# Performance work log

Hardware: AMD Instinct MI355X
Metric: run time of the kernel (lower is better)

The kernel has to match this reference:

```python
import jax, jax.numpy as jnp
import numpy as np

D = 768
HID = 4 * D
B = 16
HRES = 32
WRES = 32
T = HRES * WRES


def layernorm(x, g, b, eps=1e-5):
    m = jnp.mean(x, axis=-1, keepdims=True)
    v = jnp.mean(jnp.square(x - m), axis=-1, keepdims=True)
    return (x - m) * jax.lax.rsqrt(v + eps) * g + b


def q_shift(x, H, W):
    # Vision-RWKV quad-directional token shift: split channels into 4 groups,
    # each group takes the neighboring patch's value in one direction (zero pad).
    Bn, N, C = x.shape
    xi = x.reshape(Bn, H, W, C)
    c = C // 4
    g0 = jnp.pad(xi[:, :, :-1, 0 * c:1 * c], ((0, 0), (0, 0), (1, 0), (0, 0)))  # from left
    g1 = jnp.pad(xi[:, :, 1:, 1 * c:2 * c], ((0, 0), (0, 0), (0, 1), (0, 0)))   # from right
    g2 = jnp.pad(xi[:, :-1, :, 2 * c:3 * c], ((0, 0), (1, 0), (0, 0), (0, 0)))  # from above
    g3 = jnp.pad(xi[:, 1:, :, 3 * c:4 * c], ((0, 0), (0, 1), (0, 0), (0, 0)))   # from below
    return jnp.concatenate([g0, g1, g2, g3], axis=-1).reshape(Bn, N, C)


def wkv_scan(w_log, u, k, v):
    # Numerically stable RWKV WKV recurrence (per-channel linear attention).
    # k, v: [B, T, C]; w = -exp(w_log) is the per-channel decay, u the bonus.
    w = -jnp.exp(w_log)
    kT = jnp.swapaxes(k, 0, 1)  # [T, B, C]
    vT = jnp.swapaxes(v, 0, 1)
    Bn, C = k.shape[0], k.shape[2]
    aa0 = jnp.zeros((Bn, C), k.dtype)
    bb0 = jnp.zeros((Bn, C), k.dtype)
    pp0 = jnp.full((Bn, C), -1e30, k.dtype)

    def step(carry, kv):
        aa, bb, pp = carry
        kt, vt = kv
        ww = u + kt
        p = jnp.maximum(pp, ww)
        e1 = jnp.exp(pp - p)
        e2 = jnp.exp(ww - p)
        out = (e1 * aa + e2 * vt) / (e1 * bb + e2)
        ww2 = pp + w
        p2 = jnp.maximum(ww2, kt)
        e1b = jnp.exp(ww2 - p2)
        e2b = jnp.exp(kt - p2)
        return (e1b * aa + e2b * vt, e1b * bb + e2b, p2), out

    _, outT = jax.lax.scan(step, (aa0, bb0, pp0), (kT, vT))
    return jnp.swapaxes(outT, 0, 1)  # [B, T, C]


def setup_inputs() -> dict:
    key = jax.random.key(0)
    ks = jax.random.split(key, 16)

    def nrm(k, shape, s=0.02):
        return jax.random.normal(k, shape, jnp.float32) * s

    return {
        "x": jax.random.normal(ks[0], (B, T, D), jnp.float32),
        "H": HRES,
        "W": WRES,
        "ln1_g": jnp.ones((D,), jnp.float32),
        "ln1_b": jnp.zeros((D,), jnp.float32),
        "ln2_g": jnp.ones((D,), jnp.float32),
        "ln2_b": jnp.zeros((D,), jnp.float32),
        "mu_k": jax.random.uniform(ks[1], (D,), jnp.float32),
        "mu_v": jax.random.uniform(ks[2], (D,), jnp.float32),
        "mu_r": jax.random.uniform(ks[3], (D,), jnp.float32),
        "w_log": nrm(ks[4], (D,), 0.5),
        "u": nrm(ks[5], (D,), 0.5),
        "Wk": nrm(ks[6], (D, D)),
        "Wv": nrm(ks[7], (D, D)),
        "Wr": nrm(ks[8], (D, D)),
        "Wo": nrm(ks[9], (D, D)),
        "cmu_k": jax.random.uniform(ks[10], (D,), jnp.float32),
        "cmu_r": jax.random.uniform(ks[11], (D,), jnp.float32),
        "Ck": nrm(ks[12], (HID, D)),
        "Cv": nrm(ks[13], (D, HID)),
        "Cr": nrm(ks[14], (D, D)),
    }


def reference(x, H, W, ln1_g, ln1_b, ln2_g, ln2_b, mu_k, mu_v, mu_r, w_log, u,
              Wk, Wv, Wr, Wo, cmu_k, cmu_r, Ck, Cv, Cr):
    h = x
    # ---- spatial mix (RWKV time-mix over patch sequence) ----
    a = layernorm(h, ln1_g, ln1_b)
    sx = q_shift(a, H, W)
    xk = a * mu_k + sx * (1.0 - mu_k)
    xv = a * mu_v + sx * (1.0 - mu_v)
    xr = a * mu_r + sx * (1.0 - mu_r)
    k = xk @ Wk.T
    v = xv @ Wv.T
    r = jax.nn.sigmoid(xr @ Wr.T)
    wkv = wkv_scan(w_log, u, k, v)
    h = h + (r * wkv) @ Wo.T
    # ---- channel mix (squared-ReLU gated FFN) ----
    a2 = layernorm(h, ln2_g, ln2_b)
    sx2 = q_shift(a2, H, W)
    xk2 = a2 * cmu_k + sx2 * (1.0 - cmu_k)
    xr2 = a2 * cmu_r + sx2 * (1.0 - cmu_r)
    kk = jnp.square(jax.nn.relu(xk2 @ Ck.T))
    h = h + jax.nn.sigmoid(xr2 @ Cr.T) * (kk @ Cv.T)
    # ---- outer residual from RWKVBlock.forward ----
    return h + x
```

## Files before the change

### kernel.cpp

```cpp
#include <hip/hip_runtime.h>
#include <hip/hip_bf16.h>

#define DD   768
#define TT   1024
#define BBATCH 16
#define NROWS (BBATCH * TT)
#define HIDN 3072
#define HHALF 1536
#define HH 32
#define WW 32
#define DW  (DD * DD)
#define DH  (DD * HIDN)
#define CCH 64
#define PCH (TT / CCH)

typedef float  floatx4 __attribute__((ext_vector_type(4)));
typedef __bf16 bf16x8  __attribute__((ext_vector_type(8)));

__device__ __forceinline__ float bf2f(__hip_bfloat16 v) { return __bfloat162float(v); }
__device__ __forceinline__ __hip_bfloat16 f2bf(float v) { return __float2bfloat16(v); }
__device__ __forceinline__ float toF(__hip_bfloat16 v) { return __bfloat162float(v); }
__device__ __forceinline__ float toF(float v) { return v; }

#define GL2LDS(gp, lp)  __builtin_amdgcn_global_load_lds(                     \
    (const __attribute__((address_space(1))) void*)(gp),                      \
    (__attribute__((address_space(3))) void*)(lp), 16, 0, 0)

__global__ __launch_bounds__(256)
void cvt_k(const float* __restrict__ s, __hip_bfloat16* __restrict__ d, int n)
{
    const int i = (blockIdx.x * 256 + threadIdx.x) * 4;
    if (i >= n) return;
    const float4 v = *reinterpret_cast<const float4*>(s + i);
    __hip_bfloat16 o[4] = {f2bf(v.x), f2bf(v.y), f2bf(v.z), f2bf(v.w)};
    *reinterpret_cast<ushort4*>(d + i) = *reinterpret_cast<const ushort4*>(o);
}

template <typename TIN>
__global__ __launch_bounds__(256)
void ln_stats_k(const TIN* __restrict__ x,
                float* __restrict__ mean, float* __restrict__ rstd)
{
    const int row = blockIdx.x, tid = threadIdx.x;
    const int lane = tid & 63, wid = tid >> 6;
    const TIN* xr = x + (size_t)row * DD;
    float s1 = 0.f, s2 = 0.f;
#pragma unroll
    for (int i = 0; i < 3; ++i) {
        const float v = toF(xr[tid + i * 256]);
        s1 += v; s2 += v * v;
    }
#pragma unroll
    for (int off = 32; off > 0; off >>= 1) {
        s1 += __shfl_down(s1, off);
        s2 += __shfl_down(s2, off);
    }
    __shared__ float sh[8];
    if (lane == 0) { sh[wid] = s1; sh[4 + wid] = s2; }
    __syncthreads();
    if (tid == 0) {
        s1 = sh[0] + sh[1] + sh[2] + sh[3];
        s2 = sh[4] + sh[5] + sh[6] + sh[7];
        const float m = s1 * (1.f / DD);
        mean[row] = m;
        rstd[row] = rsqrtf(s2 * (1.f / DD) - m * m + 1e-5f);
    }
}

template <typename TIN>
__device__ __forceinline__ float ln_at(const TIN* __restrict__ x,
                                       const float* __restrict__ mean,
                                       const float* __restrict__ rstd,
                                       const float* __restrict__ g,
                                       const float* __restrict__ b,
                                       int grow, int c)
{
    return (toF(x[(size_t)grow * DD + c]) - mean[grow]) * rstd[grow] * g[c] + b[c];
}

template <typename TIN, int NOUT>
__global__ __launch_bounds__(256)
void mix_k(const TIN* __restrict__ x,
           const float* __restrict__ mean, const float* __restrict__ rstd,
           const float* __restrict__ g, const float* __restrict__ b,
           const float* __restrict__ muk,
           const float* __restrict__ muv,
           const float* __restrict__ mur,
           __hip_bfloat16* __restrict__ xk,
           __hip_bfloat16* __restrict__ xv,
           __hip_bfloat16* __restrict__ xr)
{
    const size_t idx = (size_t)blockIdx.x * 256 + threadIdx.x;
    const int c  = (int)(idx % DD);
    const int n  = (int)((idx / DD) % TT);
    const int bb = (int)(idx / ((size_t)DD * TT));
    const int y = n >> 5, xp = n & 31;
    const int grow = bb * TT + n;

    const float av = ln_at(x, mean, rstd, g, b, grow, c);

    const int grp = c / (DD / 4);
    int ny = y, nx = xp; bool ok;
    if      (grp == 0) { nx = xp - 1; ok = xp > 0;      }
    else if (grp == 1) { nx = xp + 1; ok = xp < WW - 1; }
    else if (grp == 2) { ny = y - 1;  ok = y > 0;       }
    else               { ny = y + 1;  ok = y < HH - 1;  }
    const float sx = ok ? ln_at(x, mean, rstd, g, b, bb * TT + ny * WW + nx, c) : 0.f;

    const float mk = muk[c], mr = mur[c];
    xk[idx] = f2bf(av * mk + sx * (1.f - mk));
    xr[idx] = f2bf(av * mr + sx * (1.f - mr));
    if (NOUT == 3) {
        const float mv = muv[c];
        xv[idx] = f2bf(av * mv + sx * (1.f - mv));
    }
}

#define BM 128
#define BN 128
#define BKK 64

template <int MODE>
__global__ __launch_bounds__(256, 2)
void gemm_bt(const __hip_bfloat16* __restrict__ A,
             const __hip_bfloat16* __restrict__ W,
             int K, int Wstr, int Nn,
             __hip_bfloat16* __restrict__ outB,
             float* __restrict__ outF,
             const __hip_bfloat16* __restrict__ auxS,
             const __hip_bfloat16* __restrict__ auxH,
             const float* __restrict__ auxX)
{
    __shared__ __align__(16) unsigned short lA[BM * BKK];
    __shared__ __align__(16) unsigned short lB[BN * BKK];

    const int tid  = threadIdx.x;
    const int bm   = blockIdx.x, bn = blockIdx.y;
    const int lane = tid & 63, wid = tid >> 6;
    const int l15  = lane & 15, quad = lane >> 4;
    const int m0   = (wid & 1) * 64;
    const int n0   = (wid >> 1) * 64;

    const int srow  = lane >> 3;
    const int gcolg = (lane & 7) ^ (srow & 7);
    const int s0    = wid * 4;

    floatx4 acc[4][4];
#pragma unroll
    for (int i = 0; i < 4; ++i)
#pragma unroll
        for (int j = 0; j < 4; ++j)
            acc[i][j] = floatx4{0.f, 0.f, 0.f, 0.f};

    const int swzbase = l15 & 7;

    for (int k0 = 0; k0 < K; k0 += BKK) {
#pragma unroll
        for (int t = 0; t < 4; ++t) {
            const int s   = s0 + t;
            const int row = s * 8 + srow;
            GL2LDS(A + (size_t)(bm * BM + row) * K    + k0 + gcolg * 8,
                   &lA[s * 512]);
            GL2LDS(W + (size_t)(bn * BN + row) * Wstr + k0 + gcolg * 8,
                   &lB[s * 512]);
        }
        __syncthreads();
#pragma unroll
        for (int kk = 0; kk < BKK; kk += 32) {
            const int swz = (((kk >> 3) + quad) ^ swzbase) * 8;
            bf16x8 af[4], bfr[4];
#pragma unroll
            for (int i = 0; i < 4; ++i)
                af[i] = *reinterpret_cast<const bf16x8*>(
                    &lA[(m0 + i * 16 + l15) * BKK + swz]);
#pragma unroll
            for (int j = 0; j < 4; ++j)
                bfr[j] = *reinterpret_cast<const bf16x8*>(
                    &lB[(n0 + j * 16 + l15) * BKK + swz]);
#pragma unroll
            for (int i = 0; i < 4; ++i)
#pragma unroll
                for (int j = 0; j < 4; ++j)
                    acc[i][j] = __builtin_amdgcn_mfma_f32_16x16x32_bf16(
                        af[i], bfr[j], acc[i][j], 0, 0, 0);
        }
        __syncthreads();
    }

#pragma unroll
    for (int i = 0; i < 4; ++i) {
#pragma unroll
        for (int j = 0; j < 4; ++j) {
#pragma unroll
            for (int r = 0; r < 4; ++r) {
                const int grow = bm * BM + m0 + i * 16 + quad * 4 + r;
                const int gcol = bn * BN + n0 + j * 16 + l15;
                const size_t idx = (size_t)grow * Nn + gcol;
                const float v = acc[i][j][r];
                if (MODE == 0) {
                    outB[idx] = f2bf(v);
                } else if (MODE == 1) {
                    outB[idx] = f2bf(1.f / (1.f + __expf(-v)));
                } else if (MODE == 2) {
                    outB[idx] = f2bf(v + auxX[idx]);
                } else if (MODE == 3) {
                    const float t = fmaxf(v, 0.f);
                    outB[idx] = f2bf(t * t);
                } else if (MODE == 4) {
                    outF[idx] = bf2f(auxH[idx]) + bf2f(auxS[idx]) * v + auxX[idx];
                } else {
                    outF[idx] += bf2f(auxS[idx]) * v;
                }
            }
        }
    }
}

__global__ __launch_bounds__(256)
void wkv_passA(const float* __restrict__ w_log,
               const __hip_bfloat16* __restrict__ k,
               const __hip_bfloat16* __restrict__ v,
               float* __restrict__ SA, float* __restrict__ SB,
               float* __restrict__ SP)
{
    const int c  = blockIdx.x * 256 + threadIdx.x;
    const int j  = blockIdx.y;
    const int bb = blockIdx.z;
    const float w = -__expf(w_log[c]);
    const size_t base = ((size_t)bb * TT + j * CCH) * DD + c;
    float a = 0.f, b = 0.f, p = -1e30f;
#pragma unroll 4
    for (int t = 0; t < CCH; ++t) {
        const size_t o = base + (size_t)t * DD;
        const float kt = bf2f(k[o]);
        const float vt = bf2f(v[o]);
        const float ww2 = p + w;
        const float p2  = fmaxf(ww2, kt);
        const float e1  = __expf(ww2 - p2);
        const float e2  = __expf(kt - p2);
        a = e1 * a + e2 * vt;
        b = e1 * b + e2;
        p = p2;
    }
    const size_t si = ((size_t)bb * PCH + j) * DD + c;
    SA[si] = a; SB[si] = b; SP[si] = p;
}

__global__ __launch_bounds__(256)
void wkv_scanj(const float* __restrict__ w_log,
               float* __restrict__ SA, float* __restrict__ SB,
               float* __restrict__ SP)
{
    const int idx = blockIdx.x * 256 + threadIdx.x;
    const int c = idx % DD, bb = idx / DD;
    const float wC = -__expf(w_log[c]) * (float)CCH;
    float a = 0.f, b = 0.f, p = -1e30f;
#pragma unroll
    for (int j = 0; j < PCH; ++j) {
        const size_t si = ((size_t)bb * PCH + j) * DD + c;
        const float aj = SA[si], bj = SB[si], pj = SP[si];
        SA[si] = a; SB[si] = b; SP[si] = p;
        const float pd = p + wC;
        const float pn = fmaxf(pd, pj);
        const float e1 = __expf(pd - pn);
        const float e2 = __expf(pj - pn);
        a = e1 * a + e2 * aj;
        b = e1 * b + e2 * bj;
        p = pn;
    }
}

__global__ __launch_bounds__(256)
void wkv_passB(const float* __restrict__ w_log, const float* __restrict__ u,
               const __hip_bfloat16* __restrict__ k,
               const __hip_bfloat16* __restrict__ v,
               const __hip_bfloat16* __restrict__ r,
               __hip_bfloat16* __restrict__ rw,
               const float* __restrict__ SA, const float* __restrict__ SB,
               const float* __restrict__ SP)
{
    const int c  = blockIdx.x * 256 + threadIdx.x;
    const int j  = blockIdx.y;
    const int bb = blockIdx.z;
    const float w  = -__expf(w_log[c]);
    const float uu = u[c];
    const size_t si = ((size_t)bb * PCH + j) * DD + c;
    float aa = SA[si], bbv = SB[si], pp = SP[si];
    const size_t base = ((size_t)bb * TT + j * CCH) * DD + c;
#pragma unroll 4
    for (int t = 0; t < CCH; ++t) {
        const size_t o = base + (size_t)t * DD;
        const float kt = bf2f(k[o]);
        const float vt = bf2f(v[o]);
        const float rt = bf2f(r[o]);
        const float ww = uu + kt;
        const float p  = fmaxf(pp, ww);
        const float e1 = __expf(pp - p);
        const float e2 = __expf(ww - p);
        const float ov = __fdividef(e1 * aa + e2 * vt, e1 * bbv + e2);
        rw[o] = f2bf(rt * ov);
        const float ww2 = pp + w;
        const float p2  = fmaxf(ww2, kt);
        const float e1b = __expf(ww2 - p2);
        const float e2b = __expf(kt - p2);
        aa  = e1b * aa + e2b * vt;
        bbv = e1b * bbv + e2b;
        pp  = p2;
    }
}

extern "C" void kernel_launch(void* const* d_in, const int* in_sizes, int n_in,
                              void* d_out, int out_size, void* d_ws, size_t ws_size,
                              hipStream_t stream)
{
    (void)in_sizes; (void)n_in; (void)out_size;
    const float* x     = (const float*)d_in[0];
    const float* ln1_g = (const float*)d_in[3];
    const float* ln1_b = (const float*)d_in[4];
    const float* ln2_g = (const float*)d_in[5];
    const float* ln2_b = (const float*)d_in[6];
    const float* mu_k  = (const float*)d_in[7];
    const float* mu_v  = (const float*)d_in[8];
    const float* mu_r  = (const float*)d_in[9];
    const float* w_log = (const float*)d_in[10];
    const float* u     = (const float*)d_in[11];
    const float* Wk    = (const float*)d_in[12];
    const float* Wv    = (const float*)d_in[13];
    const float* Wr    = (const float*)d_in[14];
    const float* Wo    = (const float*)d_in[15];
    const float* cmu_k = (const float*)d_in[16];
    const float* cmu_r = (const float*)d_in[17];
    const float* Ck    = (const float*)d_in[18];
    const float* Cv    = (const float*)d_in[19];
    const float* Cr    = (const float*)d_in[20];
    float* out = (float*)d_out;

    const size_t ND = (size_t)NROWS * DD;
    const size_t SL = ND * 2;
    const size_t WBYTES = (size_t)(5 * DW + 2 * DH) * 2;
    const size_t NSTATE = (size_t)BBATCH * PCH * DD;
    const size_t NEED = 5 * SL + WBYTES
                      + 2 * (size_t)NROWS * sizeof(float)
                      + 3 * NSTATE * sizeof(float);
    if (ws_size < NEED) return;

    char* w = (char*)d_ws;
    __hip_bfloat16* S0 = (__hip_bfloat16*)(w);
    __hip_bfloat16* S1 = (__hip_bfloat16*)(w + 1 * SL);
    __hip_bfloat16* S2 = (__hip_bfloat16*)(w + 2 * SL);
    __hip_bfloat16* S3 = (__hip_bfloat16*)(w + 3 * SL);
    __hip_bfloat16* S4 = (__hip_bfloat16*)(w + 4 * SL);
    __hip_bfloat16* WkB = (__hip_bfloat16*)(w + 5 * SL);
    __hip_bfloat16* WvB = WkB + DW;
    __hip_bfloat16* WrB = WvB + DW;
    __hip_bfloat16* WoB = WrB + DW;
    __hip_bfloat16* CrB = WoB + DW;
    __hip_bfloat16* CkB = CrB + DW;
    __hip_bfloat16* CvB = CkB + DH;
    float* meanB = (float*)(w + 5 * SL + WBYTES);
    float* rstdB = meanB + NROWS;
    float* SAb = rstdB + NROWS;
    float* SBb = SAb + NSTATE;
    float* SPb = SBb + NSTATE;

    const int EW_GRID = (int)(ND / 256);
    const dim3 g768(NROWS / BM, DD / BN);
    const dim3 g1536(NROWS / BM, HHALF / BN);
    const dim3 gwkv(DD / 256, PCH, BBATCH);
    const int CB_W = DW / 4 / 256;
    const int CB_H = DH / 4 / 256;

    cvt_k<<<CB_W, 256, 0, stream>>>(Wk, WkB, DW);
    cvt_k<<<CB_W, 256, 0, stream>>>(Wv, WvB, DW);
    cvt_k<<<CB_W, 256, 0, stream>>>(Wr, WrB, DW);
    cvt_k<<<CB_W, 256, 0, stream>>>(Wo, WoB, DW);
    cvt_k<<<CB_W, 256, 0, stream>>>(Cr, CrB, DW);
    cvt_k<<<CB_H, 256, 0, stream>>>(Ck, CkB, DH);
    cvt_k<<<CB_H, 256, 0, stream>>>(Cv, CvB, DH);

    ln_stats_k<float><<<NROWS, 256, 0, stream>>>(x, meanB, rstdB);
    mix_k<float, 3><<<EW_GRID, 256, 0, stream>>>(x, meanB, rstdB, ln1_g, ln1_b,
                                                 mu_k, mu_v, mu_r, S0, S1, S2);
    gemm_bt<0><<<g768, 256, 0, stream>>>(S0, WkB, DD, DD, DD, S3, nullptr, nullptr, nullptr, nullptr);
    gemm_bt<0><<<g768, 256, 0, stream>>>(S1, WvB, DD, DD, DD, S4, nullptr, nullptr, nullptr, nullptr);
    gemm_bt<1><<<g768, 256, 0, stream>>>(S2, WrB, DD, DD, DD, S0, nullptr, nullptr, nullptr, nullptr);
    wkv_passA<<<gwkv, 256, 0, stream>>>(w_log, S3, S4, SAb, SBb, SPb);
    wkv_scanj<<<(BBATCH * DD) / 256, 256, 0, stream>>>(w_log, SAb, SBb, SPb);
    wkv_passB<<<gwkv, 256, 0, stream>>>(w_log, u, S3, S4, S0, S1, SAb, SBb, SPb);
    gemm_bt<2><<<g768, 256, 0, stream>>>(S1, WoB, DD, DD, DD, S2, nullptr, nullptr, nullptr, x);

    ln_stats_k<__hip_bfloat16><<<NROWS, 256, 0, stream>>>(S2, meanB, rstdB);
    mix_k<__hip_bfloat16, 2><<<EW_GRID, 256, 0, stream>>>(S2, meanB, rstdB, ln2_g, ln2_b,
                                                          cmu_k, nullptr, cmu_r, S0, nullptr, S3);
    gemm_bt<1><<<g768, 256, 0, stream>>>(S3, CrB, DD, DD, DD, S1, nullptr, nullptr, nullptr, nullptr);
    __hip_bfloat16* kk = S3;
    gemm_bt<3><<<g1536, 256, 0, stream>>>(S0, CkB, DD, DD, HHALF,
                                          kk, nullptr, nullptr, nullptr, nullptr);
    gemm_bt<4><<<g768, 256, 0, stream>>>(kk, CvB, HHALF, HIDN, DD,
                                         nullptr, out, S1, S2, x);
    gemm_bt<3><<<g1536, 256, 0, stream>>>(S0, CkB + (size_t)HHALF * DD, DD, DD, HHALF,
                                          kk, nullptr, nullptr, nullptr, nullptr);
    gemm_bt<5><<<g768, 256, 0, stream>>>(kk, CvB + HHALF, HHALF, HIDN, DD,
                                         nullptr, out, S1, nullptr, nullptr);
}
```

Measured before the change: 614.8 us.

## Vectorize GEMM epilogues via LDS transpose, batch K/V GEMMs and weight conversions

GEMM epilogues now stage each wave's accumulator band through LDS so every lane holds 16 contiguous columns, which allows 16-byte vector loads and stores of outputs and auxiliary tensors in place of scattered 2-byte and 4-byte accesses. The K and V projections are merged into a single launch with a z-dimension, and the seven weight-conversion launches become one kernel. The goal is to cut uncoalesced epilogue memory traffic and launch overhead. The cost is extra LDS round trips in the epilogue and reuse of the GEMM tile buffer as scratch.

```diff
diff --git a/kernel.cpp b/kernel.cpp
--- a/kernel.cpp
+++ b/kernel.cpp
@@ -27,13 +27,26 @@
     (__attribute__((address_space(3))) void*)(lp), 16, 0, 0)
 
 __global__ __launch_bounds__(256)
-void cvt_k(const float* __restrict__ s, __hip_bfloat16* __restrict__ d, int n)
-{
-    const int i = (blockIdx.x * 256 + threadIdx.x) * 4;
-    if (i >= n) return;
+void cvt_all(const float* __restrict__ w0, const float* __restrict__ w1,
+             const float* __restrict__ w2, const float* __restrict__ w3,
+             const float* __restrict__ w4, const float* __restrict__ w5,
+             const float* __restrict__ w6, __hip_bfloat16* __restrict__ dst)
+{
+    const int b = blockIdx.x;
+    const float* s; size_t dofs; int rel;
+    if (b < 2880) {
+        const int seg = b / 576; rel = b - seg * 576;
+        s = seg == 0 ? w0 : seg == 1 ? w1 : seg == 2 ? w2 : seg == 3 ? w3 : w4;
+        dofs = (size_t)seg * DW;
+    } else if (b < 5184) {
+        rel = b - 2880; s = w5; dofs = 5ull * DW;
+    } else {
+        rel = b - 5184; s = w6; dofs = 5ull * DW + DH;
+    }
+    const int i = rel * 1024 + threadIdx.x * 4;
     const float4 v = *reinterpret_cast<const float4*>(s + i);
     __hip_bfloat16 o[4] = {f2bf(v.x), f2bf(v.y), f2bf(v.z), f2bf(v.w)};
-    *reinterpret_cast<ushort4*>(d + i) = *reinterpret_cast<const ushort4*>(o);
+    *reinterpret_cast<ushort4*>(&dst[dofs + i]) = *reinterpret_cast<const ushort4*>(o);
 }
 
 template <typename TIN>
@@ -120,6 +133,70 @@
 #define BN 128
 #define BKK 64
 
+__device__ __forceinline__ void gemm_core(
+    const __hip_bfloat16* __restrict__ A, const __hip_bfloat16* __restrict__ W,
+    int K, int Wstr, int bm, int bn, unsigned short* lds, floatx4 acc[4][4])
+{
+    const int tid  = threadIdx.x;
+    const int lane = tid & 63, wid = tid >> 6;
+    const int l15  = lane & 15, quad = lane >> 4;
+    const int m0   = (wid & 1) * 64;
+    const int n0   = (wid >> 1) * 64;
+    const int srow  = lane >> 3;
+    const int gcolg = (lane & 7) ^ srow;
+    const int s0    = wid * 4;
+    const int swzbase = l15 & 7;
+
+    for (int k0 = 0; k0 < K; k0 += BKK) {
+#pragma unroll
+        for (int t = 0; t < 4; ++t) {
+            const int s   = s0 + t;
+            const int row = s * 8 + srow;
+            GL2LDS(A + (size_t)(bm * BM + row) * K    + k0 + gcolg * 8,
+                   &lds[s * 512]);
+            GL2LDS(W + (size_t)(bn * BN + row) * Wstr + k0 + gcolg * 8,
+                   &lds[8192 + s * 512]);
+        }
+        __syncthreads();
+#pragma unroll
+        for (int kk = 0; kk < BKK; kk += 32) {
+            const int swz = (((kk >> 3) + quad) ^ swzbase) * 8;
+            bf16x8 af[4], bfr[4];
+#pragma unroll
+            for (int i = 0; i < 4; ++i)
+                af[i] = *reinterpret_cast<const bf16x8*>(
+                    &lds[(m0 + i * 16 + l15) * BKK + swz]);
+#pragma unroll
+            for (int j = 0; j < 4; ++j)
+                bfr[j] = *reinterpret_cast<const bf16x8*>(
+                    &lds[8192 + (n0 + j * 16 + l15) * BKK + swz]);
+#pragma unroll
+            for (int i = 0; i < 4; ++i)
+#pragma unroll
+                for (int j = 0; j < 4; ++j)
+                    acc[i][j] = __builtin_amdgcn_mfma_f32_16x16x32_bf16(
+                        af[i], bfr[j], acc[i][j], 0, 0, 0);
+        }
+        __syncthreads();
+    }
+}
+
+__device__ __forceinline__ void xpose_band(const floatx4 accRow[4], float* scr,
+                                           int lane, float cv[16])
+{
+    const int l15 = lane & 15, quad = lane >> 4;
+#pragma unroll
+    for (int j = 0; j < 4; ++j)
+#pragma unroll
+        for (int r = 0; r < 4; ++r)
+            scr[(quad * 4 + r) * 68 + j * 16 + l15] = accRow[j][r];
+    const int row_l = lane >> 2, cb = (lane & 3) * 16;
+#pragma unroll
+    for (int q = 0; q < 4; ++q)
+        *reinterpret_cast<float4*>(&cv[q * 4]) =
+            *reinterpret_cast<const float4*>(&scr[row_l * 68 + cb + q * 4]);
+}
+
 template <int MODE>
 __global__ __launch_bounds__(256, 2)
 void gemm_bt(const __hip_bfloat16* __restrict__ A,
@@ -131,19 +208,10 @@
              const __hip_bfloat16* __restrict__ auxH,
              const float* __restrict__ auxX)
 {
-    __shared__ __align__(16) unsigned short lA[BM * BKK];
-    __shared__ __align__(16) unsigned short lB[BN * BKK];
-
-    const int tid  = threadIdx.x;
-    const int bm   = blockIdx.x, bn = blockIdx.y;
-    const int lane = tid & 63, wid = tid >> 6;
-    const int l15  = lane & 15, quad = lane >> 4;
-    const int m0   = (wid & 1) * 64;
-    const int n0   = (wid >> 1) * 64;
-
-    const int srow  = lane >> 3;
-    const int gcolg = (lane & 7) ^ (srow & 7);
-    const int s0    = wid * 4;
+    __shared__ __align__(16) unsigned short lds[16384];
+    const int bm = blockIdx.x, bn = blockIdx.y;
+    const int tid = threadIdx.x, lane = tid & 63, wid = tid >> 6;
+    const int m0 = (wid & 1) * 64, n0 = (wid >> 1) * 64;
 
     floatx4 acc[4][4];
 #pragma unroll
@@ -152,67 +220,120 @@
         for (int j = 0; j < 4; ++j)
             acc[i][j] = floatx4{0.f, 0.f, 0.f, 0.f};
 
-    const int swzbase = l15 & 7;
-
-    for (int k0 = 0; k0 < K; k0 += BKK) {
-#pragma unroll
-        for (int t = 0; t < 4; ++t) {
-            const int s   = s0 + t;
-            const int row = s * 8 + srow;
-            GL2LDS(A + (size_t)(bm * BM + row) * K    + k0 + gcolg * 8,
-                   &lA[s * 512]);
-            GL2LDS(W + (size_t)(bn * BN + row) * Wstr + k0 + gcolg * 8,
-                   &lB[s * 512]);
+    gemm_core(A, W, K, Wstr, bm, bn, lds, acc);
+
+    float* scr = reinterpret_cast<float*>(lds) + wid * 1088;
+    const int row_l = lane >> 2, cb = (lane & 3) * 16;
+#pragma unroll
+    for (int i = 0; i < 4; ++i) {
+        float cv[16];
+        xpose_band(acc[i], scr, lane, cv);
+        const int grow = bm * BM + m0 + i * 16 + row_l;
+        const int gcol = bn * BN + n0 + cb;
+        const size_t idx = (size_t)grow * Nn + gcol;
+        if (MODE == 1 || MODE == 3) {
+            __hip_bfloat16 ob[16];
+#pragma unroll
+            for (int e = 0; e < 16; ++e) {
+                float v = cv[e];
+                if (MODE == 1) v = 1.f / (1.f + __expf(-v));
+                else { v = fmaxf(v, 0.f); v = v * v; }
+                ob[e] = f2bf(v);
+            }
+            *reinterpret_cast<uint4*>(&outB[idx])     = *reinterpret_cast<const uint4*>(&ob[0]);
+            *reinterpret_cast<uint4*>(&outB[idx + 8]) = *reinterpret_cast<const uint4*>(&ob[8]);
+        } else if (MODE == 2) {
+            float xv[16];
+#pragma unroll
+            for (int q = 0; q < 4; ++q)
+                *reinterpret_cast<float4*>(&xv[q * 4]) =
+                    *reinterpret_cast<const float4*>(&auxX[idx + q * 4]);
+            __hip_bfloat16 ob[16];
+#pragma unroll
+            for (int e = 0; e < 16; ++e) ob[e] = f2bf(cv[e] + xv[e]);
+            *reinterpret_cast<uint4*>(&outB[idx])     = *reinterpret_cast<const uint4*>(&ob[0]);
+            *reinterpret_cast<uint4*>(&outB[idx + 8]) = *reinterpret_cast<const uint4*>(&ob[8]);
+        } else if (MODE == 4) {
+            unsigned short hs[16], ss[16]; float xv[16], ov[16];
+            *reinterpret_cast<uint4*>(&hs[0]) = *reinterpret_cast<const uint4*>(&auxH[idx]);
+            *reinterpret_cast<uint4*>(&hs[8]) = *reinterpret_cast<const uint4*>(&auxH[idx + 8]);
+            *reinterpret_cast<uint4*>(&ss[0]) = *reinterpret_cast<const uint4*>(&auxS[idx]);
+            *reinterpret_cast<uint4*>(&ss[8]) = *reinterpret_cast<const uint4*>(&auxS[idx + 8]);
+#pragma unroll
+            for (int q = 0; q < 4; ++q)
+                *reinterpret_cast<float4*>(&xv[q * 4]) =
+                    *reinterpret_cast<const float4*>(&auxX[idx + q * 4]);
+#pragma unroll
+            for (int e = 0; e < 16; ++e)
+                ov[e] = bf2f(__hip_bfloat16_raw{hs[e]})
+                      + bf2f(__hip_bfloat16_raw{ss[e]}) * cv[e] + xv[e];
+#pragma unroll
+            for (int q = 0; q < 4; ++q)
+                *reinterpret_cast<float4*>(&outF[idx + q * 4]) =
+                    *reinterpret_cast<const float4*>(&ov[q * 4]);
+        } else {
+            unsigned short ss[16]; float ov[16];
+            *reinterpret_cast<uint4*>(&ss[0]) = *reinterpret_cast<const uint4*>(&auxS[idx]);
+            *reinterpret_cast<uint4*>(&ss[8]) = *reinterpret_cast<const uint4*>(&auxS[idx + 8]);
+#pragma unroll
+            for (int q = 0; q < 4; ++q)
+                *reinterpret_cast<float4*>(&ov[q * 4]) =
+                    *reinterpret_cast<const float4*>(&outF[idx + q * 4]);
+#pragma unroll
+            for (int e = 0; e < 16; ++e)
+                ov[e] += bf2f(__hip_bfloat16_raw{ss[e]}) * cv[e];
+#pragma unroll
+            for (int q = 0; q < 4; ++q)
+                *reinterpret_cast<float4*>(&outF[idx + q * 4]) =
+                    *reinterpret_cast<const float4*>(&ov[q * 4]);
         }
-        __syncthreads();
-#pragma unroll
-        for (int kk = 0; kk < BKK; kk += 32) {
-            const int swz = (((kk >> 3) + quad) ^ swzbase) * 8;
-            bf16x8 af[4], bfr[4];
-#pragma unroll
-            for (int i = 0; i < 4; ++i)
-                af[i] = *reinterpret_cast<const bf16x8*>(
-                    &lA[(m0 + i * 16 + l15) * BKK + swz]);
-#pragma unroll
-            for (int j = 0; j < 4; ++j)
-                bfr[j] = *reinterpret_cast<const bf16x8*>(
-                    &lB[(n0 + j * 16 + l15) * BKK + swz]);
-#pragma unroll
-            for (int i = 0; i < 4; ++i)
-#pragma unroll
-                for (int j = 0; j < 4; ++j)
-                    acc[i][j] = __builtin_amdgcn_mfma_f32_16x16x32_bf16(
-                        af[i], bfr[j], acc[i][j], 0, 0, 0);
+    }
+}
+
+__global__ __launch_bounds__(256, 2)
+void gemm_qkv(const __hip_bfloat16* __restrict__ A0, const __hip_bfloat16* __restrict__ A1,
+              const __hip_bfloat16* __restrict__ A2,
+              const __hip_bfloat16* __restrict__ W0, const __hip_bfloat16* __restrict__ W1,
+              const __hip_bfloat16* __restrict__ W2,
+              __hip_bfloat16* __restrict__ O0, __hip_bfloat16* __restrict__ O1,
+              __hip_bfloat16* __restrict__ O2)
+{
+    __shared__ __align__(16) unsigned short lds[16384];
+    const int z = blockIdx.z;
+    const __hip_bfloat16* A = z == 0 ? A0 : z == 1 ? A1 : A2;
+    const __hip_bfloat16* W = z == 0 ? W0 : z == 1 ? W1 : W2;
+    __hip_bfloat16*       O = z == 0 ? O0 : z == 1 ? O1 : O2;
+    const int bm = blockIdx.x, bn = blockIdx.y;
+    const int tid = threadIdx.x, lane = tid & 63, wid = tid >> 6;
+    const int m0 = (wid & 1) * 64, n0 = (wid >> 1) * 64;
+
+    floatx4 acc[4][4];
+#pragma unroll
+    for (int i = 0; i < 4; ++i)
+#pragma unroll
+        for (int j = 0; j < 4; ++j)
+            acc[i][j] = floatx4{0.f, 0.f, 0.f, 0.f};
+
+    gemm_core(A, W, DD, DD, bm, bn, lds, acc);
+
+    float* scr = reinterpret_cast<float*>(lds) + wid * 1088;
+    const int row_l = lane >> 2, cb = (lane & 3) * 16;
+#pragma unroll
+    for (int i = 0; i < 4; ++i) {
+        float cv[16];
+        xpose_band(acc[i], scr, lane, cv);
+        const int grow = bm * BM + m0 + i * 16 + row_l;
+        const int gcol = bn * BN + n0 + cb;
+        const size_t idx = (size_t)grow * DD + gcol;
+        __hip_bfloat16 ob[16];
+#pragma unroll
+        for (int e = 0; e < 16; ++e) {
+            float v = cv[e];
+            if (z == 2) v = 1.f / (1.f + __expf(-v));
+            ob[e] = f2bf(v);
         }
-        __syncthreads();
-    }
-
-#pragma unroll
-    for (int i = 0; i < 4; ++i) {
-#pragma unroll
-        for (int j = 0; j < 4; ++j) {
-#pragma unroll
-            for (int r = 0; r < 4; ++r) {
-                const int grow = bm * BM + m0 + i * 16 + quad * 4 + r;
-                const int gcol = bn * BN + n0 + j * 16 + l15;
-                const size_t idx = (size_t)grow * Nn + gcol;
-                const float v = acc[i][j][r];
-                if (MODE == 0) {
-                    outB[idx] = f2bf(v);
-                } else if (MODE == 1) {
-                    outB[idx] = f2bf(1.f / (1.f + __expf(-v)));
-                } else if (MODE == 2) {
-                    outB[idx] = f2bf(v + auxX[idx]);
-                } else if (MODE == 3) {
-                    const float t = fmaxf(v, 0.f);
-                    outB[idx] = f2bf(t * t);
-                } else if (MODE == 4) {
-                    outF[idx] = bf2f(auxH[idx]) + bf2f(auxS[idx]) * v + auxX[idx];
-                } else {
-                    outF[idx] += bf2f(auxS[idx]) * v;
-                }
-            }
-        }
+        *reinterpret_cast<uint4*>(&O[idx])     = *reinterpret_cast<const uint4*>(&ob[0]);
+        *reinterpret_cast<uint4*>(&O[idx + 8]) = *reinterpret_cast<const uint4*>(&ob[8]);
     }
 }
 
@@ -350,12 +471,13 @@
     __hip_bfloat16* S2 = (__hip_bfloat16*)(w + 2 * SL);
     __hip_bfloat16* S3 = (__hip_bfloat16*)(w + 3 * SL);
     __hip_bfloat16* S4 = (__hip_bfloat16*)(w + 4 * SL);
-    __hip_bfloat16* WkB = (__hip_bfloat16*)(w + 5 * SL);
-    __hip_bfloat16* WvB = WkB + DW;
-    __hip_bfloat16* WrB = WvB + DW;
-    __hip_bfloat16* WoB = WrB + DW;
-    __hip_bfloat16* CrB = WoB + DW;
-    __hip_bfloat16* CkB = CrB + DW;
+    __hip_bfloat16* WB  = (__hip_bfloat16*)(w + 5 * SL);
+    __hip_bfloat16* WkB = WB;
+    __hip_bfloat16* WvB = WB + 1ull * DW;
+    __hip_bfloat16* WrB = WB + 2ull * DW;
+    __hip_bfloat16* WoB = WB + 3ull * DW;
+    __hip_bfloat16* CrB = WB + 4ull * DW;
+    __hip_bfloat16* CkB = WB + 5ull * DW;
     __hip_bfloat16* CvB = CkB + DH;
     float* meanB = (float*)(w + 5 * SL + WBYTES);
     float* rstdB = meanB + NROWS;
@@ -366,33 +488,29 @@
     const int EW_GRID = (int)(ND / 256);
     const dim3 g768(NROWS / BM, DD / BN);
     const dim3 g1536(NROWS / BM, HHALF / BN);
+    const dim3 gqkv(NROWS / BM, DD / BN, 3);
     const dim3 gwkv(DD / 256, PCH, BBATCH);
-    const int CB_W = DW / 4 / 256;
-    const int CB_H = DH / 4 / 256;
-
-    cvt_k<<<CB_W, 256, 0, stream>>>(Wk, WkB, DW);
-    cvt_k<<<CB_W, 256, 0, stream>>>(Wv, WvB, DW);
-    cvt_k<<<CB_W, 256, 0, stream>>>(Wr, WrB, DW);
-    cvt_k<<<CB_W, 256, 0, stream>>>(Wo, WoB, DW);
-    cvt_k<<<CB_W, 256, 0, stream>>>(Cr, CrB, DW);
-    cvt_k<<<CB_H, 256, 0, stream>>>(Ck, CkB, DH);
-    cvt_k<<<CB_H, 256, 0, stream>>>(Cv, CvB, DH);
+
+    cvt_all<<<7488, 256, 0, stream>>>(Wk, Wv, Wr, Wo, Cr, Ck, Cv, WB);
 
     ln_stats_k<float><<<NROWS, 256, 0, stream>>>(x, meanB, rstdB);
     mix_k<float, 3><<<EW_GRID, 256, 0, stream>>>(x, meanB, rstdB, ln1_g, ln1_b,
                                                  mu_k, mu_v, mu_r, S0, S1, S2);
-    gemm_bt<0><<<g768, 256, 0, stream>>>(S0, WkB, DD, DD, DD, S3, nullptr, nullptr, nullptr, nullptr);
-    gemm_bt<0><<<g768, 256, 0, stream>>>(S1, WvB, DD, DD, DD, S4, nullptr, nullptr, nullptr, nullptr);
-    gemm_bt<1><<<g768, 256, 0, stream>>>(S2, WrB, DD, DD, DD, S0, nullptr, nullptr, nullptr, nullptr);
+    gemm_qkv<<<dim3(NROWS / BM, DD / BN, 2), 256, 0, stream>>>(
+        S0, S1, nullptr, WkB, WvB, nullptr, S3, S4, nullptr);
+    gemm_bt<1><<<g768, 256, 0, stream>>>(S2, WrB, DD, DD, DD, S0, nullptr,
+                                         nullptr, nullptr, nullptr);
     wkv_passA<<<gwkv, 256, 0, stream>>>(w_log, S3, S4, SAb, SBb, SPb);
     wkv_scanj<<<(BBATCH * DD) / 256, 256, 0, stream>>>(w_log, SAb, SBb, SPb);
     wkv_passB<<<gwkv, 256, 0, stream>>>(w_log, u, S3, S4, S0, S1, SAb, SBb, SPb);
-    gemm_bt<2><<<g768, 256, 0, stream>>>(S1, WoB, DD, DD, DD, S2, nullptr, nullptr, nullptr, x);
+    gemm_bt<2><<<g768, 256, 0, stream>>>(S1, WoB, DD, DD, DD, S2, nullptr,
+                                         nullptr, nullptr, x);
 
     ln_stats_k<__hip_bfloat16><<<NROWS, 256, 0, stream>>>(S2, meanB, rstdB);
     mix_k<__hip_bfloat16, 2><<<EW_GRID, 256, 0, stream>>>(S2, meanB, rstdB, ln2_g, ln2_b,
                                                           cmu_k, nullptr, cmu_r, S0, nullptr, S3);
-    gemm_bt<1><<<g768, 256, 0, stream>>>(S3, CrB, DD, DD, DD, S1, nullptr, nullptr, nullptr, nullptr);
+    gemm_bt<1><<<g768, 256, 0, stream>>>(S3, CrB, DD, DD, DD, S1, nullptr,
+                                         nullptr, nullptr, nullptr);
     __hip_bfloat16* kk = S3;
     gemm_bt<3><<<g1536, 256, 0, stream>>>(S0, CkB, DD, DD, HHALF,
                                           kk, nullptr, nullptr, nullptr, nullptr);
```

Result: faster. 580.1 us (-5.6%).
